# Kernel optimization log

Measured on AMD Instinct MI355X. Metric: run time of the kernel, lower is better.

Reference implementation:

```python
import jax, jax.numpy as jnp
import numpy as np

N, E, C = 50000, 600000, 128
BN_EPS = 1e-5
NORM_EPS = 1e-12


def _edgeconv(x, src, dst, wa, ba, g, be, rm, rv, wb, bb):
    # PyG EdgeConv: message = MLP(concat(x_i, x_j - x_i)); aggr='add' at target i
    x_i = x[dst]                      # [E, C] target features
    x_j = x[src]                      # [E, C] source features
    m = jnp.concatenate([x_i, x_j - x_i], axis=-1)   # [E, 2C]
    m = jax.nn.relu(m @ wa.T + ba)                   # Linear(2C->C) + ReLU
    m = (m - rm) * (g * jax.lax.rsqrt(rv + BN_EPS)) + be  # BatchNorm1d (eval)
    m = m @ wb.T + bb                                # Linear(C->C)
    return jax.ops.segment_sum(m, dst, num_segments=x.shape[0])  # [N, C]


def _lin(k, fan_in, shape):
    bound = 1.0 / np.sqrt(fan_in)
    return jax.random.uniform(k, shape, jnp.float32, -bound, bound)


def setup_inputs() -> dict:
    key = jax.random.key(0)
    ks = jax.random.split(key, 16)
    inp = {
        "x": jax.random.normal(ks[0], (N, C), jnp.float32),
        "edge_index": jax.random.randint(ks[1], (2, E), 0, N, jnp.int64),
    }
    # layer 1 params
    inp["w1a"] = _lin(ks[2], 2 * C, (C, 2 * C)); inp["b1a"] = _lin(ks[3], 2 * C, (C,))
    inp["g1"] = jnp.ones((C,), jnp.float32) + 0.1 * jax.random.normal(ks[4], (C,))
    inp["be1"] = 0.1 * jax.random.normal(ks[5], (C,))
    inp["rm1"] = 0.1 * jax.random.normal(ks[6], (C,))
    inp["rv1"] = 0.5 + jax.random.uniform(ks[7], (C,))
    inp["w1b"] = _lin(ks[8], C, (C, C)); inp["b1b"] = _lin(ks[9], C, (C,))
    # layer 2 params
    inp["w2a"] = _lin(ks[10], 2 * C, (C, 2 * C)); inp["b2a"] = _lin(ks[11], 2 * C, (C,))
    inp["g2"] = jnp.ones((C,), jnp.float32) + 0.1 * jax.random.normal(ks[12], (C,))
    inp["be2"] = 0.1 * jax.random.normal(ks[13], (C,))
    inp["rm2"] = 0.1 * jax.random.normal(ks[14], (C,))
    inp["rv2"] = 0.5 + jax.random.uniform(ks[15], (C,))
    k2 = jax.random.split(ks[15], 2)
    inp["w2b"] = _lin(k2[0], C, (C, C)); inp["b2b"] = _lin(k2[1], C, (C,))
    return inp


def reference(x, edge_index, w1a, b1a, g1, be1, rm1, rv1, w1b, b1b,
              w2a, b2a, g2, be2, rm2, rv2, w2b, b2b):
    src, dst = edge_index[0], edge_index[1]
    # layer 1 (all but last): conv -> relu -> L2 normalize -> dropout(eval=identity)
    h = _edgeconv(x, src, dst, w1a, b1a, g1, be1, rm1, rv1, w1b, b1b)
    h = jax.nn.relu(h)
    h = h / jnp.maximum(jnp.linalg.norm(h, axis=-1, keepdims=True), NORM_EPS)
    # last layer: conv only
    return _edgeconv(h, src, dst, w2a, b2a, g2, be2, rm2, rv2, w2b, b2b)
```

## Files before the change

kernel.cpp:

```cpp
#include <hip/hip_runtime.h>

#define CCH 128
#define WPAD 136
typedef unsigned short ushort;
typedef __attribute__((ext_vector_type(8))) short bf16x8_t;
typedef __attribute__((ext_vector_type(4))) float f32x4;

union ABu { bf16x8_t v; ushort u[8]; uint4 q; };

__device__ __forceinline__ ushort f2b(float f) {
  union { float f; unsigned u; } v{f};
  unsigned r = v.u + 0x7fffu + ((v.u >> 16) & 1u);
  return (ushort)(r >> 16);
}
__device__ __forceinline__ float b2f(ushort s) {
  union { unsigned u; float f; } v{(unsigned)s << 16};
  return v.f;
}

__global__ __launch_bounds__(256) void k_pre(const float* __restrict__ x,
                                             ushort* __restrict__ XB, int nxc,
                                             const float* __restrict__ w1a,
                                             const float* __restrict__ w1b,
                                             const float* __restrict__ w2a,
                                             const float* __restrict__ w2b,
                                             ushort* __restrict__ Wcat1, ushort* __restrict__ Wb1,
                                             ushort* __restrict__ Wcat2, ushort* __restrict__ Wb2,
                                             const void* __restrict__ ei, int* __restrict__ deg,
                                             int E, int xcb) {
  const int b = blockIdx.x, t = threadIdx.x;
  if (b < 128) {
    int i = b * 256 + t;
    int c = i >> 7, k = i & 127;
    float v = (c < 128) ? w1a[c * 256 + k] - w1a[c * 256 + 128 + k]
                        : w1a[(c - 128) * 256 + 128 + k];
    Wcat1[i] = f2b(v);
    if (i < 16384) Wb1[i] = f2b(w1b[i]);
  } else if (b < 256) {
    int i = (b - 128) * 256 + t;
    int c = i >> 7, k = i & 127;
    float v = (c < 128) ? w2a[c * 256 + k] - w2a[c * 256 + 128 + k]
                        : w2a[(c - 128) * 256 + 128 + k];
    Wcat2[i] = f2b(v);
    if (i < 16384) Wb2[i] = f2b(w2b[i]);
  } else if (b < 256 + xcb) {
    size_t i = (size_t)(b - 256) * 256 + t;
    if (i < (size_t)nxc) {
      const float* xp = x + i * 8;
      float4 f0 = *(const float4*)xp;
      float4 f1 = *(const float4*)(xp + 4);
      ushort o[8] = {f2b(f0.x), f2b(f0.y), f2b(f0.z), f2b(f0.w),
                     f2b(f1.x), f2b(f1.y), f2b(f1.z), f2b(f1.w)};
      *(uint4*)&XB[i * 8] = *(const uint4*)o;
    }
  } else {
    __shared__ int nz;
    if (t == 0) nz = 0;
    __syncthreads();
    int e = (b - 256 - xcb) * 256 + t;
    unsigned hi = (e < E) ? ((const unsigned*)ei)[2 * (size_t)e + 1] : 0u;
    if (hi) atomicAdd(&nz, 1);
    __syncthreads();
    bool i64 = (nz == 0);
    if (e < E) {
      int d = i64 ? (int)((const long long*)ei)[(size_t)E + e]
                  : ((const int*)ei)[(size_t)E + e];
      atomicAdd(&deg[d], 1);
    }
  }
}

__global__ __launch_bounds__(256) void k_rowptr(const int* __restrict__ deg,
                                                const int* __restrict__ bsum,
                                                int* __restrict__ rowptr,
                                                int n, int nb, int Etot) {
  __shared__ int s[256];
  const int t = threadIdx.x, b = blockIdx.x;
  s[t] = (t < nb && t < b) ? bsum[t] : 0;
  __syncthreads();
  for (int off = 128; off > 0; off >>= 1) {
    if (t < off) s[t] += s[t + off];
    __syncthreads();
  }
  int boffset = s[0];
  __syncthreads();
  int i = b * 256 + t;
  int v = (i < n) ? deg[i] : 0;
  s[t] = v; __syncthreads();
  for (int off = 1; off < 256; off <<= 1) {
    int tv = (t >= off) ? s[t - off] : 0;
    __syncthreads();
    s[t] += tv;
    __syncthreads();
  }
  if (i < n) rowptr[i] = boffset + s[t] - v;
  if (b == gridDim.x - 1 && t == 0) rowptr[n] = Etot;
}

__global__ __launch_bounds__(256) void k_scatter(const void* __restrict__ ei,
                                                 const int* __restrict__ rowptr,
                                                 int* __restrict__ cnt,
                                                 int* __restrict__ esrc, int E) {
  __shared__ int nz;
  const int t = threadIdx.x;
  if (t == 0) nz = 0;
  __syncthreads();
  int e = blockIdx.x * 256 + t;
  unsigned hi = (e < E) ? ((const unsigned*)ei)[2 * (size_t)e + 1] : 0u;
  if (hi) atomicAdd(&nz, 1);
  __syncthreads();
  bool i64 = (nz == 0);
  if (e < E) {
    int d, sv;
    if (i64) {
      sv = (int)((const long long*)ei)[(size_t)e];
      d  = (int)((const long long*)ei)[(size_t)E + e];
    } else {
      sv = ((const int*)ei)[(size_t)e];
      d  = ((const int*)ei)[(size_t)E + e];
    }
    int pos = rowptr[d] + atomicAdd(&cnt[d], 1);
    esrc[pos] = sv;
  }
}

__device__ __forceinline__ void gemm_core(const ushort* __restrict__ XB,
                                          const ushort* __restrict__ wlds,
                                          int rowb, int ln, int quad, int nN,
                                          f32x4 acc0[8], f32x4 acc1[8]) {
  const int ar0 = rowb + ln, ar1 = rowb + 16 + ln;
  ABu a0[4], a1[4];
#pragma unroll
  for (int kk = 0; kk < 4; ++kk) {
    a0[kk].q = (ar0 < nN) ? *(const uint4*)(XB + (size_t)ar0 * CCH + kk * 32 + quad * 8)
                          : make_uint4(0, 0, 0, 0);
    a1[kk].q = (ar1 < nN) ? *(const uint4*)(XB + (size_t)ar1 * CCH + kk * 32 + quad * 8)
                          : make_uint4(0, 0, 0, 0);
  }
#pragma unroll
  for (int s = 0; s < 8; ++s) {
    acc0[s] = (f32x4){0.f, 0.f, 0.f, 0.f};
    acc1[s] = (f32x4){0.f, 0.f, 0.f, 0.f};
  }
#pragma unroll
  for (int s = 0; s < 8; ++s) {
#pragma unroll
    for (int kk = 0; kk < 4; ++kk) {
      ABu b;
      b.q = *(const uint4*)&wlds[(s * 16 + ln) * WPAD + kk * 32 + quad * 8];
      acc0[s] = __builtin_amdgcn_mfma_f32_16x16x32_bf16(a0[kk].v, b.v, acc0[s], 0, 0, 0);
      acc1[s] = __builtin_amdgcn_mfma_f32_16x16x32_bf16(a1[kk].v, b.v, acc1[s], 0, 0, 0);
    }
  }
}

__device__ __forceinline__ void stage_w(const ushort* __restrict__ Wp,
                                        ushort* __restrict__ wlds, int t) {
  for (int i = t; i < 128 * 16; i += 256) {
    int row = i >> 4, ch = i & 15;
    *(uint4*)&wlds[row * WPAD + ch * 8] = *(const uint4*)&Wp[row * CCH + ch * 8];
  }
}

__device__ __forceinline__ void epi0(f32x4 acc[8], int rowb, int ln, int quad, int nN,
                                     const float* bias, int half, ushort* dst) {
#pragma unroll
  for (int s = 0; s < 8; ++s) {
    int col = s * 16 + ln;
    float bv = half ? 0.f : bias[col];
#pragma unroll
    for (int r = 0; r < 4; ++r) {
      int row = rowb + quad * 4 + r;
      if (row < nN) dst[(size_t)row * CCH + col] = f2b(acc[s][r] + bv);
    }
  }
}

__global__ __launch_bounds__(256) void k_mix1(const ushort* __restrict__ XB,
                                              const ushort* __restrict__ Wcat,
                                              const float* __restrict__ bias,
                                              ushort* __restrict__ A1,
                                              ushort* __restrict__ A2, int nN,
                                              const int* __restrict__ deg,
                                              int* __restrict__ bsum, int gH, int n) {
  __shared__ ushort wlds[128 * WPAD];
  const int t = threadIdx.x;
  if ((int)blockIdx.x >= 2 * gH) {
    int* s = (int*)wlds;
    int bb = blockIdx.x - 2 * gH;
    int i = bb * 256 + t;
    s[t] = (i < n) ? deg[i] : 0;
    __syncthreads();
    for (int off = 128; off > 0; off >>= 1) {
      if (t < off) s[t] += s[t + off];
      __syncthreads();
    }
    if (t == 0) bsum[bb] = s[0];
    return;
  }
  const int half = (int)blockIdx.x >= gH;
  const int bx = half ? blockIdx.x - gH : blockIdx.x;
  stage_w(Wcat + (size_t)half * 128 * CCH, wlds, t);
  __syncthreads();
  const int wave = t >> 6, lane = t & 63;
  const int ln = lane & 15, quad = lane >> 4;
  const int rowb = bx * 128 + wave * 32;
  f32x4 acc0[8], acc1[8];
  gemm_core(XB, wlds, rowb, ln, quad, nN, acc0, acc1);
  ushort* dst = half ? A2 : A1;
  epi0(acc0, rowb, ln, quad, nN, bias, half, dst);
  epi0(acc1, rowb + 16, ln, quad, nN, bias, half, dst);
}

template <int EPI>
__global__ __launch_bounds__(256) void k_gemm(const ushort* __restrict__ XB,
                                              const ushort* __restrict__ W,
                                              const float* __restrict__ bias,
                                              const int* __restrict__ deg,
                                              void* __restrict__ Y1,
                                              ushort* __restrict__ Y2, int nN) {
  __shared__ ushort wlds[128 * WPAD];
  const int t = threadIdx.x;
  const int half = (EPI == 0) ? blockIdx.y : 0;
  stage_w(W + (size_t)half * 128 * CCH, wlds, t);
  __syncthreads();
  const int wave = t >> 6, lane = t & 63;
  const int ln = lane & 15, quad = lane >> 4;
  const int rowb = blockIdx.x * 128 + wave * 32;
  f32x4 acc0[8], acc1[8];
  gemm_core(XB, wlds, rowb, ln, quad, nN, acc0, acc1);

  if constexpr (EPI == 0) {
    ushort* dst = half ? Y2 : (ushort*)Y1;
    epi0(acc0, rowb, ln, quad, nN, bias, half, dst);
    epi0(acc1, rowb + 16, ln, quad, nN, bias, half, dst);
  } else if constexpr (EPI == 1) {
    ushort* H = (ushort*)Y1;
    float biasv[8];
#pragma unroll
    for (int s = 0; s < 8; ++s) biasv[s] = bias[s * 16 + ln];
    auto epi = [&](f32x4* acc, int rb) {
#pragma unroll
      for (int r = 0; r < 4; ++r) {
        int row = rb + quad * 4 + r;
        float dn = (row < nN) ? (float)deg[row] : 0.f;
        float vals[8];
        float ss = 0.f;
#pragma unroll
        for (int s = 0; s < 8; ++s) {
          float v = fmaxf(acc[s][r] + dn * biasv[s], 0.f);
          vals[s] = v;
          ss += v * v;
        }
        ss += __shfl_xor(ss, 1, 64);
        ss += __shfl_xor(ss, 2, 64);
        ss += __shfl_xor(ss, 4, 64);
        ss += __shfl_xor(ss, 8, 64);
        float inv = 1.0f / fmaxf(sqrtf(ss), 1e-12f);
        if (row < nN) {
#pragma unroll
          for (int s = 0; s < 8; ++s)
            H[(size_t)row * CCH + s * 16 + ln] = f2b(vals[s] * inv);
        }
      }
    };
    epi(acc0, rowb); epi(acc1, rowb + 16);
  } else {
    float* OUT = (float*)Y1;
    float biasv[8];
#pragma unroll
    for (int s = 0; s < 8; ++s) biasv[s] = bias[s * 16 + ln];
    auto epi = [&](f32x4* acc, int rb) {
#pragma unroll
      for (int r = 0; r < 4; ++r) {
        int row = rb + quad * 4 + r;
        if (row >= nN) continue;
        float dn = (float)deg[row];
#pragma unroll
        for (int s = 0; s < 8; ++s)
          OUT[(size_t)row * CCH + s * 16 + ln] = acc[s][r] + dn * biasv[s];
      }
    };
    epi(acc0, rowb); epi(acc1, rowb + 16);
  }
}

__global__ __launch_bounds__(256) void k_aggr(const ushort* __restrict__ A1,
                                              const ushort* __restrict__ A2,
                                              const int* __restrict__ rowptr,
                                              const int* __restrict__ esrc,
                                              const float* __restrict__ g,
                                              const float* __restrict__ be,
                                              const float* __restrict__ rm,
                                              const float* __restrict__ rv,
                                              ushort* __restrict__ M, int nNodes) {
  int node = blockIdx.x * 4 + (threadIdx.x >> 6);
  if (node >= nNodes) return;
  int lane = threadIdx.x & 63;
  int q = lane >> 4;
  int c = (lane & 15) * 8;

  uint4 aq = *(const uint4*)&A1[(size_t)node * CCH + c];
  float a[8] = {b2f((ushort)aq.x), b2f((ushort)(aq.x >> 16)),
                b2f((ushort)aq.y), b2f((ushort)(aq.y >> 16)),
                b2f((ushort)aq.z), b2f((ushort)(aq.z >> 16)),
                b2f((ushort)aq.w), b2f((ushort)(aq.w >> 16))};
  int r0 = rowptr[node], r1 = rowptr[node + 1];
  float s[8] = {0.f, 0.f, 0.f, 0.f, 0.f, 0.f, 0.f, 0.f};

  auto acc8 = [&](uint4 w) {
    const unsigned* p = (const unsigned*)&w;
#pragma unroll
    for (int j = 0; j < 4; ++j) {
      s[2*j]   += fmaxf(a[2*j]   + b2f((ushort)p[j]), 0.f);
      s[2*j+1] += fmaxf(a[2*j+1] + b2f((ushort)(p[j] >> 16)), 0.f);
    }
  };

  for (int base = r0; base < r1; base += 64) {
    int navail = r1 - base; if (navail > 64) navail = 64;
    int myi = (lane < navail) ? esrc[base + lane] : 0;
    int g4 = navail >> 2, tail = navail & 3;
    int j = 0;
    for (; j + 4 <= g4; j += 4) {
      int p0 = j * 4 + q;
      int i0 = __shfl(myi, p0, 64);
      int i1 = __shfl(myi, p0 + 4, 64);
      int i2 = __shfl(myi, p0 + 8, 64);
      int i3 = __shfl(myi, p0 + 12, 64);
      uint4 w0 = *(const uint4*)&A2[(size_t)i0 * CCH + c];
      uint4 w1 = *(const uint4*)&A2[(size_t)i1 * CCH + c];
      uint4 w2 = *(const uint4*)&A2[(size_t)i2 * CCH + c];
      uint4 w3 = *(const uint4*)&A2[(size_t)i3 * CCH + c];
      acc8(w0); acc8(w1); acc8(w2); acc8(w3);
    }
    for (; j < g4; ++j) {
      int i0 = __shfl(myi, j * 4 + q, 64);
      acc8(*(const uint4*)&A2[(size_t)i0 * CCH + c]);
    }
    int pt = g4 * 4 + q; if (pt > 63) pt = 63;
    int it = __shfl(myi, pt, 64);
    if (q < tail) acc8(*(const uint4*)&A2[(size_t)it * CCH + c]);
  }
#pragma unroll
  for (int j = 0; j < 8; ++j) {
    s[j] += __shfl_xor(s[j], 16, 64);
    s[j] += __shfl_xor(s[j], 32, 64);
  }

  if (q == 0) {
    float dn = (float)(r1 - r0);
    unsigned p[4];
#pragma unroll
    for (int j = 0; j < 4; ++j) {
      float sc0 = g[c + 2*j]     * rsqrtf(rv[c + 2*j]     + 1e-5f);
      float sc1 = g[c + 2*j + 1] * rsqrtf(rv[c + 2*j + 1] + 1e-5f);
      float o0 = sc0 * s[2*j]     + dn * (be[c + 2*j]     - rm[c + 2*j]     * sc0);
      float o1 = sc1 * s[2*j + 1] + dn * (be[c + 2*j + 1] - rm[c + 2*j + 1] * sc1);
      p[j] = (unsigned)f2b(o0) | ((unsigned)f2b(o1) << 16);
    }
    *(uint4*)&M[(size_t)node * CCH + c] = make_uint4(p[0], p[1], p[2], p[3]);
  }
}

extern "C" void kernel_launch(void* const* d_in, const int* in_sizes, int n_in,
                              void* d_out, int out_size, void* d_ws, size_t ws_size,
                              hipStream_t stream) {
  const float* x   = (const float*)d_in[0];
  const void*  ei  = d_in[1];
  const float* w1a = (const float*)d_in[2];
  const float* b1a = (const float*)d_in[3];
  const float* g1  = (const float*)d_in[4];
  const float* be1 = (const float*)d_in[5];
  const float* rm1 = (const float*)d_in[6];
  const float* rv1 = (const float*)d_in[7];
  const float* w1b = (const float*)d_in[8];
  const float* b1b = (const float*)d_in[9];
  const float* w2a = (const float*)d_in[10];
  const float* b2a = (const float*)d_in[11];
  const float* g2  = (const float*)d_in[12];
  const float* be2 = (const float*)d_in[13];
  const float* rm2 = (const float*)d_in[14];
  const float* rv2 = (const float*)d_in[15];
  const float* w2b = (const float*)d_in[16];
  const float* b2b = (const float*)d_in[17];

  const int N = in_sizes[0] / CCH;
  const int E = in_sizes[1] / 2;
  const size_t NC = (size_t)N * CCH;

  int* deg    = (int*)d_ws;
  int* cnt    = deg + N;
  int* rowptr = cnt + N;
  int* bsum   = rowptr + N + 1;
  int* esrc   = bsum + 256;
  uintptr_t pw = ((uintptr_t)(esrc + E) + 63) & ~(uintptr_t)63;
  ushort* Wcat1 = (ushort*)pw;
  ushort* Wcat2 = Wcat1 + 32768;
  ushort* Wb1   = Wcat2 + 32768;
  ushort* Wb2   = Wb1 + 16384;
  uintptr_t pb = ((uintptr_t)(Wb2 + 16384) + 63) & ~(uintptr_t)63;
  ushort* XB = (ushort*)pb;
  ushort* B0 = XB + NC;
  ushort* B1 = B0 + NC;
  ushort* MB = B1 + NC;
  ushort* HB = MB + NC;

  const int gE  = (E + 255) / 256;
  const int gS  = (N + 255) / 256;
  const int gH  = (N + 127) / 128;
  const int gA  = (N + 3) / 4;
  const int nxc = (int)(NC / 8);
  const int xcb = (nxc + 255) / 256;

  hipMemsetAsync(deg, 0, sizeof(int) * 2 * (size_t)N, stream);
  k_pre<<<256 + xcb + gE, 256, 0, stream>>>(x, XB, nxc, w1a, w1b, w2a, w2b,
                                            Wcat1, Wb1, Wcat2, Wb2, ei, deg, E, xcb);
  k_mix1<<<2 * gH + gS, 256, 0, stream>>>(XB, Wcat1, b1a, B0, B1, N, deg, bsum, gH, N);
  k_rowptr<<<gS, 256, 0, stream>>>(deg, bsum, rowptr, N, gS, E);
  k_scatter<<<gE, 256, 0, stream>>>(ei, rowptr, cnt, esrc, E);

  k_aggr<<<gA, 256, 0, stream>>>(B0, B1, rowptr, esrc, g1, be1, rm1, rv1, MB, N);
  k_gemm<1><<<gH, 256, 0, stream>>>(MB, Wb1, b1b, deg, HB, nullptr, N);
  k_gemm<0><<<dim3(gH, 2), 256, 0, stream>>>(HB, Wcat2, b2a, deg, B0, B1, N);
  k_aggr<<<gA, 256, 0, stream>>>(B0, B1, rowptr, esrc, g2, be2, rm2, rv2, MB, N);
  k_gemm<2><<<gH, 256, 0, stream>>>(MB, Wb2, b2b, deg, d_out, nullptr, N);
}
```

Before: 299.9 us.

## Fuse layer-1 output GEMM with layer-2 input GEMM and convert x in-kernel

Fuses the layer-1 Linear+ReLU+L2-normalize GEMM with the layer-2 concat-weight GEMM into one kernel that keeps the normalized rows in shared memory, removing the HB intermediate round trip and one launch. The fp32-to-bf16 conversion of x moves into the first mix GEMM's operand load, dropping the separate XB buffer pass. rowptr now also initializes cnt so the scatter needs one fewer load and the memset shrinks. GEMM kernels process one 16-row accumulator set at a time, lowering register pressure. The cost is that the fused kernel restages weights twice per block with extra syncs, using 64-row tiles.

```diff
diff --git a/kernel.cpp b/kernel.cpp
--- a/kernel.cpp
+++ b/kernel.cpp
@@ -18,16 +18,14 @@
   return v.f;
 }
 
-__global__ __launch_bounds__(256) void k_pre(const float* __restrict__ x,
-                                             ushort* __restrict__ XB, int nxc,
-                                             const float* __restrict__ w1a,
+__global__ __launch_bounds__(256) void k_pre(const float* __restrict__ w1a,
                                              const float* __restrict__ w1b,
                                              const float* __restrict__ w2a,
                                              const float* __restrict__ w2b,
                                              ushort* __restrict__ Wcat1, ushort* __restrict__ Wb1,
                                              ushort* __restrict__ Wcat2, ushort* __restrict__ Wb2,
                                              const void* __restrict__ ei, int* __restrict__ deg,
-                                             int E, int xcb) {
+                                             int E) {
   const int b = blockIdx.x, t = threadIdx.x;
   if (b < 128) {
     int i = b * 256 + t;
@@ -43,21 +41,11 @@
                         : w2a[(c - 128) * 256 + 128 + k];
     Wcat2[i] = f2b(v);
     if (i < 16384) Wb2[i] = f2b(w2b[i]);
-  } else if (b < 256 + xcb) {
-    size_t i = (size_t)(b - 256) * 256 + t;
-    if (i < (size_t)nxc) {
-      const float* xp = x + i * 8;
-      float4 f0 = *(const float4*)xp;
-      float4 f1 = *(const float4*)(xp + 4);
-      ushort o[8] = {f2b(f0.x), f2b(f0.y), f2b(f0.z), f2b(f0.w),
-                     f2b(f1.x), f2b(f1.y), f2b(f1.z), f2b(f1.w)};
-      *(uint4*)&XB[i * 8] = *(const uint4*)o;
-    }
   } else {
     __shared__ int nz;
     if (t == 0) nz = 0;
     __syncthreads();
-    int e = (b - 256 - xcb) * 256 + t;
+    int e = (b - 256) * 256 + t;
     unsigned hi = (e < E) ? ((const unsigned*)ei)[2 * (size_t)e + 1] : 0u;
     if (hi) atomicAdd(&nz, 1);
     __syncthreads();
@@ -73,6 +61,7 @@
 __global__ __launch_bounds__(256) void k_rowptr(const int* __restrict__ deg,
                                                 const int* __restrict__ bsum,
                                                 int* __restrict__ rowptr,
+                                                int* __restrict__ cnt,
                                                 int n, int nb, int Etot) {
   __shared__ int s[256];
   const int t = threadIdx.x, b = blockIdx.x;
@@ -93,12 +82,15 @@
     s[t] += tv;
     __syncthreads();
   }
-  if (i < n) rowptr[i] = boffset + s[t] - v;
+  if (i < n) {
+    int rp = boffset + s[t] - v;
+    rowptr[i] = rp;
+    cnt[i] = rp;
+  }
   if (b == gridDim.x - 1 && t == 0) rowptr[n] = Etot;
 }
 
 __global__ __launch_bounds__(256) void k_scatter(const void* __restrict__ ei,
-                                                 const int* __restrict__ rowptr,
                                                  int* __restrict__ cnt,
                                                  int* __restrict__ esrc, int E) {
   __shared__ int nz;
@@ -119,38 +111,8 @@
       sv = ((const int*)ei)[(size_t)e];
       d  = ((const int*)ei)[(size_t)E + e];
     }
-    int pos = rowptr[d] + atomicAdd(&cnt[d], 1);
+    int pos = atomicAdd(&cnt[d], 1);
     esrc[pos] = sv;
-  }
-}
-
-__device__ __forceinline__ void gemm_core(const ushort* __restrict__ XB,
-                                          const ushort* __restrict__ wlds,
-                                          int rowb, int ln, int quad, int nN,
-                                          f32x4 acc0[8], f32x4 acc1[8]) {
-  const int ar0 = rowb + ln, ar1 = rowb + 16 + ln;
-  ABu a0[4], a1[4];
-#pragma unroll
-  for (int kk = 0; kk < 4; ++kk) {
-    a0[kk].q = (ar0 < nN) ? *(const uint4*)(XB + (size_t)ar0 * CCH + kk * 32 + quad * 8)
-                          : make_uint4(0, 0, 0, 0);
-    a1[kk].q = (ar1 < nN) ? *(const uint4*)(XB + (size_t)ar1 * CCH + kk * 32 + quad * 8)
-                          : make_uint4(0, 0, 0, 0);
-  }
-#pragma unroll
-  for (int s = 0; s < 8; ++s) {
-    acc0[s] = (f32x4){0.f, 0.f, 0.f, 0.f};
-    acc1[s] = (f32x4){0.f, 0.f, 0.f, 0.f};
-  }
-#pragma unroll
-  for (int s = 0; s < 8; ++s) {
-#pragma unroll
-    for (int kk = 0; kk < 4; ++kk) {
-      ABu b;
-      b.q = *(const uint4*)&wlds[(s * 16 + ln) * WPAD + kk * 32 + quad * 8];
-      acc0[s] = __builtin_amdgcn_mfma_f32_16x16x32_bf16(a0[kk].v, b.v, acc0[s], 0, 0, 0);
-      acc1[s] = __builtin_amdgcn_mfma_f32_16x16x32_bf16(a1[kk].v, b.v, acc1[s], 0, 0, 0);
-    }
   }
 }
 
@@ -162,6 +124,21 @@
   }
 }
 
+__device__ __forceinline__ void mfma8(const ABu a[4], const ushort* __restrict__ wlds,
+                                      int ln, int quad, f32x4 acc[8]) {
+#pragma unroll
+  for (int s = 0; s < 8; ++s) acc[s] = (f32x4){0.f, 0.f, 0.f, 0.f};
+#pragma unroll
+  for (int s = 0; s < 8; ++s) {
+#pragma unroll
+    for (int kk = 0; kk < 4; ++kk) {
+      ABu b;
+      b.q = *(const uint4*)&wlds[(s * 16 + ln) * WPAD + kk * 32 + quad * 8];
+      acc[s] = __builtin_amdgcn_mfma_f32_16x16x32_bf16(a[kk].v, b.v, acc[s], 0, 0, 0);
+    }
+  }
+}
+
 __device__ __forceinline__ void epi0(f32x4 acc[8], int rowb, int ln, int quad, int nN,
                                      const float* bias, int half, ushort* dst) {
 #pragma unroll
@@ -176,7 +153,7 @@
   }
 }
 
-__global__ __launch_bounds__(256) void k_mix1(const ushort* __restrict__ XB,
+__global__ __launch_bounds__(256) void k_mix1(const float* __restrict__ X,
                                               const ushort* __restrict__ Wcat,
                                               const float* __restrict__ bias,
                                               ushort* __restrict__ A1,
@@ -205,84 +182,140 @@
   const int wave = t >> 6, lane = t & 63;
   const int ln = lane & 15, quad = lane >> 4;
   const int rowb = bx * 128 + wave * 32;
-  f32x4 acc0[8], acc1[8];
-  gemm_core(XB, wlds, rowb, ln, quad, nN, acc0, acc1);
+
+  ABu a0[4], a1[4];
+#pragma unroll
+  for (int kk = 0; kk < 4; ++kk) {
+    auto ldc = [&](int r, ABu& d) {
+      if (r < nN) {
+        const float* xp = X + (size_t)r * CCH + kk * 32 + quad * 8;
+        float4 f0 = *(const float4*)xp;
+        float4 f1 = *(const float4*)(xp + 4);
+        d.u[0] = f2b(f0.x); d.u[1] = f2b(f0.y); d.u[2] = f2b(f0.z); d.u[3] = f2b(f0.w);
+        d.u[4] = f2b(f1.x); d.u[5] = f2b(f1.y); d.u[6] = f2b(f1.z); d.u[7] = f2b(f1.w);
+      } else d.q = make_uint4(0, 0, 0, 0);
+    };
+    ldc(rowb + ln, a0[kk]); ldc(rowb + 16 + ln, a1[kk]);
+  }
+  f32x4 acc[8];
   ushort* dst = half ? A2 : A1;
-  epi0(acc0, rowb, ln, quad, nN, bias, half, dst);
-  epi0(acc1, rowb + 16, ln, quad, nN, bias, half, dst);
-}
-
-template <int EPI>
-__global__ __launch_bounds__(256) void k_gemm(const ushort* __restrict__ XB,
-                                              const ushort* __restrict__ W,
-                                              const float* __restrict__ bias,
-                                              const int* __restrict__ deg,
-                                              void* __restrict__ Y1,
-                                              ushort* __restrict__ Y2, int nN) {
+  mfma8(a0, wlds, ln, quad, acc);
+  epi0(acc, rowb, ln, quad, nN, bias, half, dst);
+  mfma8(a1, wlds, ln, quad, acc);
+  epi0(acc, rowb + 16, ln, quad, nN, bias, half, dst);
+}
+
+__global__ __launch_bounds__(256) void k_fuse2(const ushort* __restrict__ M,
+                                               const ushort* __restrict__ Wb,
+                                               const float* __restrict__ bb,
+                                               const int* __restrict__ deg,
+                                               const ushort* __restrict__ Wcat,
+                                               const float* __restrict__ ba2,
+                                               ushort* __restrict__ A1,
+                                               ushort* __restrict__ A2, int nN) {
+  __shared__ ushort wlds[128 * WPAD];
+  __shared__ ushort hs[4 * 16 * WPAD];
+  const int t = threadIdx.x;
+  const int wave = t >> 6, lane = t & 63;
+  const int ln = lane & 15, quad = lane >> 4;
+  const int rowb = blockIdx.x * 64 + wave * 16;
+  ushort* hw = &hs[wave * 16 * WPAD];
+
+  stage_w(Wb, wlds, t);
+  __syncthreads();
+  {
+    const int arow = rowb + ln;
+    ABu a[4];
+#pragma unroll
+    for (int kk = 0; kk < 4; ++kk)
+      a[kk].q = (arow < nN) ? *(const uint4*)(M + (size_t)arow * CCH + kk * 32 + quad * 8)
+                            : make_uint4(0, 0, 0, 0);
+    f32x4 acc[8];
+    mfma8(a, wlds, ln, quad, acc);
+    float biasv[8];
+#pragma unroll
+    for (int s = 0; s < 8; ++s) biasv[s] = bb[s * 16 + ln];
+#pragma unroll
+    for (int r = 0; r < 4; ++r) {
+      int row = rowb + quad * 4 + r;
+      float dn = (row < nN) ? (float)deg[row] : 0.f;
+      float vals[8];
+      float ss = 0.f;
+#pragma unroll
+      for (int s = 0; s < 8; ++s) {
+        float v = fmaxf(acc[s][r] + dn * biasv[s], 0.f);
+        vals[s] = v;
+        ss += v * v;
+      }
+      ss += __shfl_xor(ss, 1, 64);
+      ss += __shfl_xor(ss, 2, 64);
+      ss += __shfl_xor(ss, 4, 64);
+      ss += __shfl_xor(ss, 8, 64);
+      float inv = 1.0f / fmaxf(sqrtf(ss), 1e-12f);
+      int lr = quad * 4 + r;
+#pragma unroll
+      for (int s = 0; s < 8; ++s) hw[lr * WPAD + s * 16 + ln] = f2b(vals[s] * inv);
+    }
+  }
+  ABu ha[4];
+#pragma unroll
+  for (int kk = 0; kk < 4; ++kk)
+    ha[kk].q = *(const uint4*)&hw[ln * WPAD + kk * 32 + quad * 8];
+
+  __syncthreads();
+  stage_w(Wcat, wlds, t);
+  __syncthreads();
+  f32x4 acc[8];
+  mfma8(ha, wlds, ln, quad, acc);
+  epi0(acc, rowb, ln, quad, nN, ba2, 0, A1);
+
+  __syncthreads();
+  stage_w(Wcat + (size_t)128 * CCH, wlds, t);
+  __syncthreads();
+  mfma8(ha, wlds, ln, quad, acc);
+  epi0(acc, rowb, ln, quad, nN, ba2, 1, A2);
+}
+
+__global__ __launch_bounds__(256) void k_gemm2(const ushort* __restrict__ M,
+                                               const ushort* __restrict__ W,
+                                               const float* __restrict__ bias,
+                                               const int* __restrict__ deg,
+                                               float* __restrict__ OUT, int nN) {
   __shared__ ushort wlds[128 * WPAD];
   const int t = threadIdx.x;
-  const int half = (EPI == 0) ? blockIdx.y : 0;
-  stage_w(W + (size_t)half * 128 * CCH, wlds, t);
+  stage_w(W, wlds, t);
   __syncthreads();
   const int wave = t >> 6, lane = t & 63;
   const int ln = lane & 15, quad = lane >> 4;
   const int rowb = blockIdx.x * 128 + wave * 32;
-  f32x4 acc0[8], acc1[8];
-  gemm_core(XB, wlds, rowb, ln, quad, nN, acc0, acc1);
-
-  if constexpr (EPI == 0) {
-    ushort* dst = half ? Y2 : (ushort*)Y1;
-    epi0(acc0, rowb, ln, quad, nN, bias, half, dst);
-    epi0(acc1, rowb + 16, ln, quad, nN, bias, half, dst);
-  } else if constexpr (EPI == 1) {
-    ushort* H = (ushort*)Y1;
-    float biasv[8];
-#pragma unroll
-    for (int s = 0; s < 8; ++s) biasv[s] = bias[s * 16 + ln];
-    auto epi = [&](f32x4* acc, int rb) {
-#pragma unroll
-      for (int r = 0; r < 4; ++r) {
-        int row = rb + quad * 4 + r;
-        float dn = (row < nN) ? (float)deg[row] : 0.f;
-        float vals[8];
-        float ss = 0.f;
-#pragma unroll
-        for (int s = 0; s < 8; ++s) {
-          float v = fmaxf(acc[s][r] + dn * biasv[s], 0.f);
-          vals[s] = v;
-          ss += v * v;
-        }
-        ss += __shfl_xor(ss, 1, 64);
-        ss += __shfl_xor(ss, 2, 64);
-        ss += __shfl_xor(ss, 4, 64);
-        ss += __shfl_xor(ss, 8, 64);
-        float inv = 1.0f / fmaxf(sqrtf(ss), 1e-12f);
-        if (row < nN) {
-#pragma unroll
-          for (int s = 0; s < 8; ++s)
-            H[(size_t)row * CCH + s * 16 + ln] = f2b(vals[s] * inv);
-        }
-      }
-    };
-    epi(acc0, rowb); epi(acc1, rowb + 16);
-  } else {
-    float* OUT = (float*)Y1;
-    float biasv[8];
-#pragma unroll
-    for (int s = 0; s < 8; ++s) biasv[s] = bias[s * 16 + ln];
-    auto epi = [&](f32x4* acc, int rb) {
-#pragma unroll
-      for (int r = 0; r < 4; ++r) {
-        int row = rb + quad * 4 + r;
-        if (row >= nN) continue;
-        float dn = (float)deg[row];
-#pragma unroll
-        for (int s = 0; s < 8; ++s)
-          OUT[(size_t)row * CCH + s * 16 + ln] = acc[s][r] + dn * biasv[s];
-      }
-    };
-    epi(acc0, rowb); epi(acc1, rowb + 16);
-  }
+
+  ABu a0[4], a1[4];
+#pragma unroll
+  for (int kk = 0; kk < 4; ++kk) {
+    int r0 = rowb + ln, r1 = rowb + 16 + ln;
+    a0[kk].q = (r0 < nN) ? *(const uint4*)(M + (size_t)r0 * CCH + kk * 32 + quad * 8)
+                         : make_uint4(0, 0, 0, 0);
+    a1[kk].q = (r1 < nN) ? *(const uint4*)(M + (size_t)r1 * CCH + kk * 32 + quad * 8)
+                         : make_uint4(0, 0, 0, 0);
+  }
+  float biasv[8];
+#pragma unroll
+  for (int s = 0; s < 8; ++s) biasv[s] = bias[s * 16 + ln];
+
+  f32x4 acc[8];
+  auto epi = [&](f32x4* ac, int rb) {
+#pragma unroll
+    for (int r = 0; r < 4; ++r) {
+      int row = rb + quad * 4 + r;
+      if (row >= nN) continue;
+      float dn = (float)deg[row];
+#pragma unroll
+      for (int s = 0; s < 8; ++s)
+        OUT[(size_t)row * CCH + s * 16 + ln] = ac[s][r] + dn * biasv[s];
+    }
+  };
+  mfma8(a0, wlds, ln, quad, acc); epi(acc, rowb);
+  mfma8(a1, wlds, ln, quad, acc); epi(acc, rowb + 16);
 }
 
 __global__ __launch_bounds__(256) void k_aggr(const ushort* __restrict__ A1,
@@ -400,29 +433,25 @@
   ushort* Wb1   = Wcat2 + 32768;
   ushort* Wb2   = Wb1 + 16384;
   uintptr_t pb = ((uintptr_t)(Wb2 + 16384) + 63) & ~(uintptr_t)63;
-  ushort* XB = (ushort*)pb;
-  ushort* B0 = XB + NC;
+  ushort* B0 = (ushort*)pb;
   ushort* B1 = B0 + NC;
   ushort* MB = B1 + NC;
-  ushort* HB = MB + NC;
 
   const int gE  = (E + 255) / 256;
   const int gS  = (N + 255) / 256;
   const int gH  = (N + 127) / 128;
+  const int gF  = (N + 63) / 64;
   const int gA  = (N + 3) / 4;
-  const int nxc = (int)(NC / 8);
-  const int xcb = (nxc + 255) / 256;
-
-  hipMemsetAsync(deg, 0, sizeof(int) * 2 * (size_t)N, stream);
-  k_pre<<<256 + xcb + gE, 256, 0, stream>>>(x, XB, nxc, w1a, w1b, w2a, w2b,
-                                            Wcat1, Wb1, Wcat2, Wb2, ei, deg, E, xcb);
-  k_mix1<<<2 * gH + gS, 256, 0, stream>>>(XB, Wcat1, b1a, B0, B1, N, deg, bsum, gH, N);
-  k_rowptr<<<gS, 256, 0, stream>>>(deg, bsum, rowptr, N, gS, E);
-  k_scatter<<<gE, 256, 0, stream>>>(ei, rowptr, cnt, esrc, E);
+
+  hipMemsetAsync(deg, 0, sizeof(int) * (size_t)N, stream);
+  k_pre<<<256 + gE, 256, 0, stream>>>(w1a, w1b, w2a, w2b,
+                                      Wcat1, Wb1, Wcat2, Wb2, ei, deg, E);
+  k_mix1<<<2 * gH + gS, 256, 0, stream>>>(x, Wcat1, b1a, B0, B1, N, deg, bsum, gH, N);
+  k_rowptr<<<gS, 256, 0, stream>>>(deg, bsum, rowptr, cnt, N, gS, E);
+  k_scatter<<<gE, 256, 0, stream>>>(ei, cnt, esrc, E);
 
   k_aggr<<<gA, 256, 0, stream>>>(B0, B1, rowptr, esrc, g1, be1, rm1, rv1, MB, N);
-  k_gemm<1><<<gH, 256, 0, stream>>>(MB, Wb1, b1b, deg, HB, nullptr, N);
-  k_gemm<0><<<dim3(gH, 2), 256, 0, stream>>>(HB, Wcat2, b2a, deg, B0, B1, N);
+  k_fuse2<<<gF, 256, 0, stream>>>(MB, Wb1, b1b, deg, Wcat2, b2a, B0, B1, N);
   k_aggr<<<gA, 256, 0, stream>>>(B0, B1, rowptr, esrc, g2, be2, rm2, rv2, MB, N);
-  k_gemm<2><<<gH, 256, 0, stream>>>(MB, Wb2, b2b, deg, d_out, nullptr, N);
-}
+  k_gemm2<<<gH, 256, 0, stream>>>(MB, Wb2, b2b, deg, (float*)d_out, N);
+}
```

After: 318.9 us. 1.06x slower.
